# Kernel optimization log

Hardware: AMD Instinct MI355X
Metric: run time of the kernel (lower is better)

The kernel has to match this reference:

```python
import jax, jax.numpy as jnp
import numpy as np

D = 64        # in_out_dim
M = 512       # hidden_dim
N = 4096      # batch
R = 10        # rank of quadratic term A (min(10, d+1))
ALPHA0 = 1.0  # alpha[0]
H = 1.0       # ResNet step h = 1/(nTh-1), nTh=2


def antideriv_tanh(x):
    # log(2*cosh(x)), numerically stable antiderivative of tanh
    ax = jnp.abs(x)
    return ax + jnp.log1p(jnp.exp(-2.0 * ax))


def setup_inputs() -> dict:
    key = jax.random.key(0)
    ks = jax.random.split(key, 10)
    f32 = jnp.float32
    return {
        "x":   jax.random.normal(ks[0], (N, D), f32),
        "t":   jax.random.uniform(ks[1], (), f32),
        "K0":  jax.random.normal(ks[2], (M, D + 1), f32) * (1.0 / np.sqrt(D + 1)),
        "b0":  jax.random.normal(ks[3], (M,), f32) * 0.1,
        "K1":  jax.random.normal(ks[4], (M, M), f32) * (1.0 / np.sqrt(M)),
        "b1":  jax.random.normal(ks[5], (M,), f32) * 0.1,
        "w":   jax.random.normal(ks[6], (M,), f32) * (1.0 / np.sqrt(M)),
        "A":   jax.random.normal(ks[7], (R, D + 1), f32) * (1.0 / np.sqrt(D + 1)),
        "c_w": jax.random.normal(ks[8], (D + 1,), f32) * 0.1,
        "c_b": jax.random.normal(ks[9], (), f32) * 0.1,
    }


def _tr_hess(s, K0, b0, K1, b1, w, A, c_w):
    # s: [N, d+1]; analytic gradient + Hessian trace of the OT-Flow potential.
    d = s.shape[1] - 1
    symA = A.T @ A                                   # [d+1, d+1]

    # forward through ResNet (nTh=2 -> one residual layer)
    opening = s @ K0.T + b0                          # [N, m]
    u0 = antideriv_tanh(opening)                     # [N, m]
    lin1 = u0 @ K1.T + b1                            # [N, m]

    tanh_open = jnp.tanh(opening)
    tanh_lin1 = jnp.tanh(lin1)

    # backward z-chain for the gradient
    z1 = w + H * (tanh_lin1 * w) @ K1                # [N, m]
    z0 = (tanh_open * z1) @ K0                       # [N, d+1]
    grad = z0 + s @ symA + c_w                       # [N, d+1]

    # trace of Hessian w.r.t. the first d coordinates
    Kopen = K0[:, :d]                                # [m, d]
    dt_open = 1.0 - tanh_open ** 2
    trH = (dt_open * z1) @ jnp.sum(Kopen ** 2, axis=1)          # [N]
    Jac = tanh_open[:, :, None] * Kopen[None]                    # [N, m, d]
    KJ = jnp.einsum('ij,njk->nik', K1, Jac)                      # [N, m, d]
    dt_lin1 = 1.0 - tanh_lin1 ** 2
    t1 = jnp.einsum('nj,njk->n', dt_lin1 * w, KJ ** 2)           # [N]
    trH = trH + H * t1 + jnp.trace(symA[:d, :d])
    return grad, trH


def reference(x, t, K0, b0, K1, b1, w, A, c_w, c_b):
    n = x.shape[0]
    s = jnp.concatenate([x, jnp.ones((n, 1), x.dtype) * t], axis=1)  # pad time
    gradPhi, trH = _tr_hess(s, K0, b0, K1, b1, w, A, c_w)
    dPhi_dx = gradPhi[:, :D]                         # [N, d]
    dPhi_dt = gradPhi[:, D:D + 1]                    # [N, 1]
    dz_dt = -(1.0 / ALPHA0) * dPhi_dx
    dlogp_dt = -(1.0 / ALPHA0) * trH[:, None]
    cost_L_dt = 0.5 * jnp.sum(dz_dt ** 2, axis=1, keepdims=True)
    cost_HJB_dt = jnp.abs(-dPhi_dt + ALPHA0 * cost_L_dt)
    return (dz_dt, dlogp_dt, cost_L_dt, cost_HJB_dt)
```

## Files before the change

### kernel.cpp

```cpp
#include <hip/hip_runtime.h>
#include <stdint.h>

#define D_  64
#define DP1 65
#define M_  512
#define N_  4096

typedef float f32x4 __attribute__((ext_vector_type(4)));
typedef _Float16 h8 __attribute__((ext_vector_type(8)));

__global__ void prepk(const float* __restrict__ A, const float* __restrict__ K0,
                      const float* __restrict__ K1, const float* __restrict__ x,
                      const float* __restrict__ tptr, const float* __restrict__ b0,
                      float* symA, float* sumK2,
                      _Float16* K1h, _Float16* K1Th, _Float16* K0Th,
                      _Float16* u0h, _Float16* ah, float* trH0){
  __shared__ float shm[2*64*66];
  int b = blockIdx.x;
  int t = threadIdx.x;
  if (b == 0){
    for (int idx = t; idx < DP1*DP1; idx += 256){
      int e = idx / DP1, d = idx % DP1;
      float s = 0.f;
      for (int r = 0; r < 10; ++r) s += A[r*DP1+e]*A[r*DP1+d];
      symA[idx] = s;
    }
    for (int m = t; m < M_; m += 256){
      float s = 0.f;
      for (int k = 0; k < D_; ++k){ float v = K0[m*DP1+k]; s += v*v; }
      sumK2[m] = s;
    }
  } else if (b < 65){
    int bb = b - 1;
    int r0 = (bb>>3)*64, c0 = (bb&7)*64;
    float* tile = shm;
    for (int it = 0; it < 16; ++it){
      int lin = it*256 + t;
      int r = lin >> 6, c = lin & 63;
      float v = K1[(r0+r)*M_ + c0+c];
      tile[r*65+c] = v;
      K1h[(r0+r)*M_ + c0+c] = (_Float16)v;
    }
    __syncthreads();
    for (int it = 0; it < 16; ++it){
      int lin = it*256 + t;
      int r = lin >> 6, c = lin & 63;
      K1Th[(c0+r)*M_ + (r0+c)] = (_Float16)tile[c*65+r];
    }
  } else if (b < 225){
    int idx = (b-65)*256 + t;
    if (idx < 80*M_){
      int d = idx / M_, i = idx % M_;
      float v = (d < DP1) ? K0[i*DP1 + d] : 0.f;
      K0Th[idx] = (_Float16)v;
    }
  } else {
    int bb = b - 225;
    int n0 = (bb & 63)*64, m0 = (bb >> 6)*64;
    float* sS = shm;
    float* sK = shm + 64*66;
    float tval = tptr[0];
    for (int it = 0; it < 17; ++it){
      int lin = it*256 + t;
      if (lin < 64*65){
        int r = lin/65, c = lin%65;
        sS[r*66+c] = (c < 64) ? x[(n0+r)*64 + c] : tval;
        sK[r*66+c] = K0[(m0+r)*DP1 + c];
      }
    }
    __syncthreads();
    int tn = (t>>4)*4, tm = (t&15)*4;
    float acc[4][4] = {};
    for (int e = 0; e < DP1; ++e){
      float sv[4], kv[4];
      for (int i=0;i<4;++i){ sv[i]=sS[(tn+i)*66+e]; kv[i]=sK[(tm+i)*66+e]; }
      for (int i=0;i<4;++i) for(int j=0;j<4;++j) acc[i][j] += sv[i]*kv[j];
    }
    for (int i=0;i<4;++i) for(int j=0;j<4;++j){
      int n = n0+tn+i, m = m0+tm+j;
      float o = acc[i][j] + b0[m];
      float a = tanhf(o);
      float ax = fabsf(o);
      float u0 = ax + log1pf(expf(-2.f*ax));
      u0h[n*M_+m] = (_Float16)u0;
      ah[n*M_+m]  = (_Float16)a;
    }
    if (m0 == 0 && t < 64) trH0[n0+t] = 0.f;
  }
}

template<int MODE>
__launch_bounds__(256, 2)
__global__ void gemm512(const _Float16* __restrict__ Ah, const _Float16* __restrict__ Wh,
                        const float* __restrict__ bias, const float* __restrict__ w,
                        const _Float16* __restrict__ ah, const float* __restrict__ sumK2,
                        _Float16* out0, _Float16* out1, float* trH0){
  __shared__ _Float16 sW[64*512];
  int n0 = blockIdx.x*64, i0 = blockIdx.y*64;
  int t = threadIdx.x;
  int wv = t>>6, l = t&63;
  int c15 = l & 15, g = l>>4;
  h8 af[16];
  {
    const _Float16* ap = Ah + (size_t)(n0 + wv*16 + c15)*M_ + g*8;
    #pragma unroll
    for (int tt = 0; tt < 16; ++tt) af[tt] = *(const h8*)(ap + tt*32);
  }
  #pragma unroll
  for (int it = 0; it < 16; ++it){
    int r = it*4 + wv;
    const _Float16* src = Wh + (size_t)(i0 + r)*M_ + ((l ^ (r & 7))*8);
    __builtin_amdgcn_global_load_lds(
        (const __attribute__((address_space(1))) void*)src,
        (__attribute__((address_space(3))) void*)(&sW[r*512]), 16, 0, 0);
  }
  __syncthreads();
  f32x4 zero = {0.f,0.f,0.f,0.f};
  f32x4 acc[4]; for (int k=0;k<4;++k) acc[k]=zero;
  #pragma unroll
  for (int step = 0; step < 16; ++step){
    int p0 = (((step*4 + g) ^ (c15 & 7))*8);
    h8 bf0 = *(const h8*)(&sW[(     c15)*512 + p0]);
    h8 bf1 = *(const h8*)(&sW[(16 + c15)*512 + p0]);
    h8 bf2 = *(const h8*)(&sW[(32 + c15)*512 + p0]);
    h8 bf3 = *(const h8*)(&sW[(48 + c15)*512 + p0]);
    h8 a = af[step];
    acc[0] = __builtin_amdgcn_mfma_f32_16x16x32_f16(a, bf0, acc[0], 0, 0, 0);
    acc[1] = __builtin_amdgcn_mfma_f32_16x16x32_f16(a, bf1, acc[1], 0, 0, 0);
    acc[2] = __builtin_amdgcn_mfma_f32_16x16x32_f16(a, bf2, acc[2], 0, 0, 0);
    acc[3] = __builtin_amdgcn_mfma_f32_16x16x32_f16(a, bf3, acc[3], 0, 0, 0);
  }
  if (MODE == 0){
    for (int kt=0;kt<4;++kt) for (int r=0;r<4;++r){
      int n = n0+wv*16+(l>>4)*4+r;
      int i = i0+kt*16+c15;
      float v = acc[kt][r] + bias[i];
      float tl = tanhf(v);
      out0[n*M_+i] = (_Float16)(tl*w[i]);
      out1[n*M_+i] = (_Float16)((1.f-tl*tl)*w[i]);
    }
  } else {
    for (int r=0;r<4;++r){
      int n = n0+wv*16+(l>>4)*4+r;
      float rowpart = 0.f;
      for (int kt=0;kt<4;++kt){
        int i = i0+kt*16+c15;
        float z1 = acc[kt][r] + w[i];
        float a = (float)ah[n*M_+i];
        out0[n*M_+i] = (_Float16)(a*z1);
        rowpart += (1.f-a*a)*z1*sumK2[i];
      }
      for (int m=1;m<16;m<<=1) rowpart += __shfl_xor(rowpart, m);
      if (c15==0) atomicAdd(&trH0[n], rowpart);
    }
  }
}

__launch_bounds__(256, 4)
__global__ void gemmz0(const _Float16* __restrict__ az1h, const _Float16* __restrict__ K0Th,
                       float* z0p){
  int n0 = blockIdx.x*64;
  int q  = blockIdx.y;
  int t = threadIdx.x, wv = t>>6, l = t&63;
  int r15 = l & 15;
  int krow = q*128 + (l>>4)*8;
  const _Float16* abase = az1h + (size_t)(n0 + wv*16 + r15)*M_ + krow;
  const _Float16* kb0 = K0Th + (size_t)( 0 + r15)*M_ + krow;
  const _Float16* kb1 = K0Th + (size_t)(16 + r15)*M_ + krow;
  const _Float16* kb2 = K0Th + (size_t)(32 + r15)*M_ + krow;
  const _Float16* kb3 = K0Th + (size_t)(48 + r15)*M_ + krow;
  const _Float16* kb4 = K0Th + (size_t)(64 + r15)*M_ + krow;
  f32x4 zero = {0.f,0.f,0.f,0.f};
  f32x4 acc[5]; for (int k=0;k<5;++k) acc[k]=zero;
  #pragma unroll
  for (int ii = 0; ii < 4; ++ii){
    const int j0 = ii*32;
    h8 af = *(const h8*)(abase + j0);
    h8 b0c = *(const h8*)(kb0 + j0);
    h8 b1c = *(const h8*)(kb1 + j0);
    h8 b2c = *(const h8*)(kb2 + j0);
    h8 b3c = *(const h8*)(kb3 + j0);
    h8 b4c = *(const h8*)(kb4 + j0);
    acc[0] = __builtin_amdgcn_mfma_f32_16x16x32_f16(af, b0c, acc[0], 0, 0, 0);
    acc[1] = __builtin_amdgcn_mfma_f32_16x16x32_f16(af, b1c, acc[1], 0, 0, 0);
    acc[2] = __builtin_amdgcn_mfma_f32_16x16x32_f16(af, b2c, acc[2], 0, 0, 0);
    acc[3] = __builtin_amdgcn_mfma_f32_16x16x32_f16(af, b3c, acc[3], 0, 0, 0);
    acc[4] = __builtin_amdgcn_mfma_f32_16x16x32_f16(af, b4c, acc[4], 0, 0, 0);
  }
  float* zp = z0p + (size_t)q*N_*80;
  for (int dt=0; dt<5; ++dt) for (int r=0;r<4;++r){
    int n = n0+wv*16+(l>>4)*4+r;
    int d = dt*16+r15;
    zp[n*80+d] = acc[dt][r];
  }
}

__launch_bounds__(256, 2)
__global__ void kjk13(const _Float16* __restrict__ K1h, const _Float16* __restrict__ K0Th,
                      const _Float16* __restrict__ ah, const _Float16* __restrict__ ch,
                      float* trH0){
  __shared__ _Float16 sK1[64*512];
  __shared__ _Float16 sAv[8*512];
  int t = threadIdx.x;
  int n0 = blockIdx.x*8;
  int i0 = blockIdx.y*64;
  int wv = t>>6, l = t&63;
  int c15 = l & 15, g = l>>4;
  h8 kf[16];
  {
    const _Float16* kfp = K0Th + (size_t)(wv*16 + c15)*M_ + g*8;
    #pragma unroll
    for (int tt = 0; tt < 16; ++tt) kf[tt] = *(const h8*)(kfp + tt*32);
  }
  #pragma unroll
  for (int it = 0; it < 16; ++it){
    int r = it*4 + wv;
    const _Float16* src = K1h + (size_t)(i0 + r)*M_ + ((l ^ (r & 7))*8);
    __builtin_amdgcn_global_load_lds(
        (const __attribute__((address_space(1))) void*)src,
        (__attribute__((address_space(3))) void*)(&sK1[r*512]), 16, 0, 0);
  }
  #pragma unroll
  for (int it = 0; it < 2; ++it){
    int cc = it*256 + t;
    int s = cc >> 6, c = cc & 63;
    *(h8*)(&sAv[s*512 + c*8]) = *(const h8*)(ah + (size_t)(n0+s)*M_ + c*8);
  }
  __syncthreads();
  f32x4 zero = {0.f,0.f,0.f,0.f};
  f32x4 acc[4][8];
  #pragma unroll
  for (int tt=0;tt<4;++tt)
    #pragma unroll
    for (int s=0;s<8;++s) acc[tt][s]=zero;
  #pragma unroll
  for (int step = 0; step < 16; ++step){
    int p0 = (((step*4 + g) ^ (c15 & 7))*8);
    h8 bf0 = *(const h8*)(&sK1[(     c15)*512 + p0]);
    h8 bf1 = *(const h8*)(&sK1[(16 + c15)*512 + p0]);
    h8 bf2 = *(const h8*)(&sK1[(32 + c15)*512 + p0]);
    h8 bf3 = *(const h8*)(&sK1[(48 + c15)*512 + p0]);
    int aoff = step*32 + g*8;
    h8 k = kf[step];
    #pragma unroll
    for (int s = 0; s < 8; ++s){
      h8 av = *(const h8*)(&sAv[s*512 + aoff]);
      h8 ap = k*av;
      acc[0][s] = __builtin_amdgcn_mfma_f32_16x16x32_f16(ap, bf0, acc[0][s], 0, 0, 0);
      acc[1][s] = __builtin_amdgcn_mfma_f32_16x16x32_f16(ap, bf1, acc[1][s], 0, 0, 0);
      acc[2][s] = __builtin_amdgcn_mfma_f32_16x16x32_f16(ap, bf2, acc[2][s], 0, 0, 0);
      acc[3][s] = __builtin_amdgcn_mfma_f32_16x16x32_f16(ap, bf3, acc[3][s], 0, 0, 0);
    }
  }
  #pragma unroll
  for (int s = 0; s < 8; ++s){
    float part = 0.f;
    #pragma unroll
    for (int tt = 0; tt < 4; ++tt){
      float ci = (float)ch[(size_t)(n0+s)*M_ + i0 + tt*16 + c15];
      f32x4 a = acc[tt][s];
      part += ci*(a[0]*a[0] + a[1]*a[1] + a[2]*a[2] + a[3]*a[3]);
    }
    for (int m=32;m>=1;m>>=1) part += __shfl_xor(part, m);
    if (l == 0) atomicAdd(&trH0[n0+s], part);
  }
}

__global__ void finalk(const float* __restrict__ x, const float* __restrict__ tptr,
                       const float* __restrict__ symA, const float* __restrict__ c_w,
                       const float* __restrict__ z0p, const float* __restrict__ trH0,
                       float* out){
  __shared__ float sA[DP1*DP1];
  int t = threadIdx.x;
  for (int i = t; i < DP1*DP1; i += 256) sA[i] = symA[i];
  __syncthreads();
  int wv = t>>6, l = t&63;
  int n = blockIdx.x*4 + wv;
  float tval = tptr[0];
  float sv = x[n*64 + l];
  float z0l = z0p[(size_t)0*N_*80 + n*80 + l] + z0p[(size_t)1*N_*80 + n*80 + l]
            + z0p[(size_t)2*N_*80 + n*80 + l] + z0p[(size_t)3*N_*80 + n*80 + l];
  float z0t = z0p[(size_t)0*N_*80 + n*80 + 64] + z0p[(size_t)1*N_*80 + n*80 + 64]
            + z0p[(size_t)2*N_*80 + n*80 + 64] + z0p[(size_t)3*N_*80 + n*80 + 64];
  float acc = z0l + c_w[l];
  for (int e = 0; e < 64; ++e){
    float se = __shfl(sv, e);
    acc += se * sA[l*DP1 + e];
  }
  acc += tval * sA[l*DP1 + 64];
  float trd = sA[l*66];
  for (int m=32;m>=1;m>>=1) trd += __shfl_xor(trd, m);
  float g64 = sv * sA[64*DP1 + l];
  for (int m=32;m>=1;m>>=1) g64 += __shfl_xor(g64, m);
  g64 += tval*sA[64*DP1+64] + z0t + c_w[64];
  float dz = -acc;
  out[n*64 + l] = dz;
  float q = dz*dz;
  for (int m=32;m>=1;m>>=1) q += __shfl_xor(q, m);
  float costL = 0.5f*q;
  if (l == 0){
    out[N_*64 + n]        = -(trH0[n] + trd);
    out[N_*64 + N_ + n]   = costL;
    out[N_*64 + 2*N_ + n] = fabsf(-g64 + costL);
  }
}

extern "C" void kernel_launch(void* const* d_in, const int* in_sizes, int n_in,
                              void* d_out, int out_size, void* d_ws, size_t ws_size,
                              hipStream_t stream){
  const float* x   = (const float*)d_in[0];
  const float* tp  = (const float*)d_in[1];
  const float* K0  = (const float*)d_in[2];
  const float* b0  = (const float*)d_in[3];
  const float* K1  = (const float*)d_in[4];
  const float* b1  = (const float*)d_in[5];
  const float* w   = (const float*)d_in[6];
  const float* A   = (const float*)d_in[7];
  const float* c_w = (const float*)d_in[8];
  float* out = (float*)d_out;

  char* ws = (char*)d_ws;
  size_t off = 0;
  auto alloc = [&](size_t bytes)->void*{
    void* p = ws + off; off += bytes; off = (off + 255) & ~(size_t)255; return p;
  };
  _Float16* K1h   = (_Float16*)alloc(512*512*2);
  _Float16* K1Th  = (_Float16*)alloc(512*512*2);
  _Float16* K0Th  = (_Float16*)alloc(80*512*2);
  float* symA     = (float*)alloc(DP1*DP1*4);
  float* sumK2    = (float*)alloc(512*4);
  _Float16* u0h   = (_Float16*)alloc((size_t)N_*M_*2);
  _Float16* ah    = (_Float16*)alloc((size_t)N_*M_*2);
  _Float16* tl1wh = (_Float16*)alloc((size_t)N_*M_*2);
  _Float16* ch    = (_Float16*)alloc((size_t)N_*M_*2);
  _Float16* az1h  = (_Float16*)alloc((size_t)N_*M_*2);
  float* z0p      = (float*)alloc((size_t)4*N_*80*4);
  float* trH0     = (float*)alloc(N_*4);

  prepk<<<737, 256, 0, stream>>>(A, K0, K1, x, tp, b0, symA, sumK2,
                                 K1h, K1Th, K0Th, u0h, ah, trH0);
  gemm512<0><<<dim3(N_/64, M_/64), 256, 0, stream>>>(u0h, K1h, b1, w, nullptr, nullptr,
                                                     tl1wh, ch, nullptr);
  gemm512<1><<<dim3(N_/64, M_/64), 256, 0, stream>>>(tl1wh, K1Th, nullptr, w, ah, sumK2,
                                                     az1h, nullptr, trH0);
  gemmz0<<<dim3(N_/64, 4), 256, 0, stream>>>(az1h, K0Th, z0p);
  kjk13<<<dim3(N_/8, 8), 256, 0, stream>>>(K1h, K0Th, ah, ch, trH0);
  finalk<<<N_/4, 256, 0, stream>>>(x, tp, symA, c_w, z0p, trH0, out);
}
```

Baseline: 193.0 us.

## Merge second GEMM with KJ trace kernel and fold z0 GEMM into final kernel

The independent gemm512<1> and kjk13 launches become one combined grid, with block index choosing the role, so their work can overlap on the GPU. The separate gemmz0 MFMA kernel and its partial-sum buffer are removed. finalk now computes z0 itself as scalar fp16 dot products over the 512-wide hidden dimension. This removes two launches and the z0p round trip, but moves a 4096x512x65 product from MFMA onto per-lane scalar loops that read K0Th rows with a poor access pattern.

```diff
diff --git a/kernel.cpp b/kernel.cpp
--- a/kernel.cpp
+++ b/kernel.cpp
@@ -89,12 +89,10 @@
   }
 }
 
-template<int MODE>
 __launch_bounds__(256, 2)
-__global__ void gemm512(const _Float16* __restrict__ Ah, const _Float16* __restrict__ Wh,
-                        const float* __restrict__ bias, const float* __restrict__ w,
-                        const _Float16* __restrict__ ah, const float* __restrict__ sumK2,
-                        _Float16* out0, _Float16* out1, float* trH0){
+__global__ void gemm0(const _Float16* __restrict__ Ah, const _Float16* __restrict__ Wh,
+                      const float* __restrict__ bias, const float* __restrict__ w,
+                      _Float16* out0, _Float16* out1){
   __shared__ _Float16 sW[64*512];
   int n0 = blockIdx.x*64, i0 = blockIdx.y*64;
   int t = threadIdx.x;
@@ -130,16 +128,124 @@
     acc[2] = __builtin_amdgcn_mfma_f32_16x16x32_f16(a, bf2, acc[2], 0, 0, 0);
     acc[3] = __builtin_amdgcn_mfma_f32_16x16x32_f16(a, bf3, acc[3], 0, 0, 0);
   }
-  if (MODE == 0){
-    for (int kt=0;kt<4;++kt) for (int r=0;r<4;++r){
-      int n = n0+wv*16+(l>>4)*4+r;
-      int i = i0+kt*16+c15;
-      float v = acc[kt][r] + bias[i];
-      float tl = tanhf(v);
-      out0[n*M_+i] = (_Float16)(tl*w[i]);
-      out1[n*M_+i] = (_Float16)((1.f-tl*tl)*w[i]);
+  for (int kt=0;kt<4;++kt) for (int r=0;r<4;++r){
+    int n = n0+wv*16+(l>>4)*4+r;
+    int i = i0+kt*16+c15;
+    float v = acc[kt][r] + bias[i];
+    float tl = tanhf(v);
+    out0[n*M_+i] = (_Float16)(tl*w[i]);
+    out1[n*M_+i] = (_Float16)((1.f-tl*tl)*w[i]);
+  }
+}
+
+__launch_bounds__(256, 2)
+__global__ void g1kjk(const _Float16* __restrict__ tl1wh, const _Float16* __restrict__ K1Th,
+                      const _Float16* __restrict__ K1h, const _Float16* __restrict__ K0Th,
+                      const _Float16* __restrict__ ah, const _Float16* __restrict__ ch,
+                      const float* __restrict__ w, const float* __restrict__ sumK2,
+                      _Float16* az1h, float* trH0){
+  __shared__ _Float16 shm[64*512 + 8*512];
+  int b = blockIdx.x;
+  int t = threadIdx.x;
+  int wv = t>>6, l = t&63;
+  int c15 = l & 15, g = l>>4;
+  if (b < 4096){
+    _Float16* sK1 = shm;
+    _Float16* sAv = shm + 64*512;
+    int n0 = (b>>3)*8;
+    int i0 = (b&7)*64;
+    h8 kf[16];
+    {
+      const _Float16* kfp = K0Th + (size_t)(wv*16 + c15)*M_ + g*8;
+      #pragma unroll
+      for (int tt = 0; tt < 16; ++tt) kf[tt] = *(const h8*)(kfp + tt*32);
+    }
+    #pragma unroll
+    for (int it = 0; it < 16; ++it){
+      int r = it*4 + wv;
+      const _Float16* src = K1h + (size_t)(i0 + r)*M_ + ((l ^ (r & 7))*8);
+      __builtin_amdgcn_global_load_lds(
+          (const __attribute__((address_space(1))) void*)src,
+          (__attribute__((address_space(3))) void*)(&sK1[r*512]), 16, 0, 0);
+    }
+    #pragma unroll
+    for (int it = 0; it < 2; ++it){
+      int cc = it*256 + t;
+      int s = cc >> 6, c = cc & 63;
+      *(h8*)(&sAv[s*512 + c*8]) = *(const h8*)(ah + (size_t)(n0+s)*M_ + c*8);
+    }
+    __syncthreads();
+    f32x4 zero = {0.f,0.f,0.f,0.f};
+    f32x4 acc[4][8];
+    #pragma unroll
+    for (int tt=0;tt<4;++tt)
+      #pragma unroll
+      for (int s=0;s<8;++s) acc[tt][s]=zero;
+    #pragma unroll
+    for (int step = 0; step < 16; ++step){
+      int p0 = (((step*4 + g) ^ (c15 & 7))*8);
+      h8 bf0 = *(const h8*)(&sK1[(     c15)*512 + p0]);
+      h8 bf1 = *(const h8*)(&sK1[(16 + c15)*512 + p0]);
+      h8 bf2 = *(const h8*)(&sK1[(32 + c15)*512 + p0]);
+      h8 bf3 = *(const h8*)(&sK1[(48 + c15)*512 + p0]);
+      int aoff = step*32 + g*8;
+      h8 k = kf[step];
+      #pragma unroll
+      for (int s = 0; s < 8; ++s){
+        h8 av = *(const h8*)(&sAv[s*512 + aoff]);
+        h8 ap = k*av;
+        acc[0][s] = __builtin_amdgcn_mfma_f32_16x16x32_f16(ap, bf0, acc[0][s], 0, 0, 0);
+        acc[1][s] = __builtin_amdgcn_mfma_f32_16x16x32_f16(ap, bf1, acc[1][s], 0, 0, 0);
+        acc[2][s] = __builtin_amdgcn_mfma_f32_16x16x32_f16(ap, bf2, acc[2][s], 0, 0, 0);
+        acc[3][s] = __builtin_amdgcn_mfma_f32_16x16x32_f16(ap, bf3, acc[3][s], 0, 0, 0);
+      }
+    }
+    #pragma unroll
+    for (int s = 0; s < 8; ++s){
+      float part = 0.f;
+      #pragma unroll
+      for (int tt = 0; tt < 4; ++tt){
+        float ci = (float)ch[(size_t)(n0+s)*M_ + i0 + tt*16 + c15];
+        f32x4 a = acc[tt][s];
+        part += ci*(a[0]*a[0] + a[1]*a[1] + a[2]*a[2] + a[3]*a[3]);
+      }
+      for (int m=32;m>=1;m>>=1) part += __shfl_xor(part, m);
+      if (l == 0) atomicAdd(&trH0[n0+s], part);
     }
   } else {
+    _Float16* sW = shm;
+    int bb = b - 4096;
+    int n0 = (bb>>3)*64, i0 = (bb&7)*64;
+    h8 af[16];
+    {
+      const _Float16* ap = tl1wh + (size_t)(n0 + wv*16 + c15)*M_ + g*8;
+      #pragma unroll
+      for (int tt = 0; tt < 16; ++tt) af[tt] = *(const h8*)(ap + tt*32);
+    }
+    #pragma unroll
+    for (int it = 0; it < 16; ++it){
+      int r = it*4 + wv;
+      const _Float16* src = K1Th + (size_t)(i0 + r)*M_ + ((l ^ (r & 7))*8);
+      __builtin_amdgcn_global_load_lds(
+          (const __attribute__((address_space(1))) void*)src,
+          (__attribute__((address_space(3))) void*)(&sW[r*512]), 16, 0, 0);
+    }
+    __syncthreads();
+    f32x4 zero = {0.f,0.f,0.f,0.f};
+    f32x4 acc[4]; for (int k=0;k<4;++k) acc[k]=zero;
+    #pragma unroll
+    for (int step = 0; step < 16; ++step){
+      int p0 = (((step*4 + g) ^ (c15 & 7))*8);
+      h8 bf0 = *(const h8*)(&sW[(     c15)*512 + p0]);
+      h8 bf1 = *(const h8*)(&sW[(16 + c15)*512 + p0]);
+      h8 bf2 = *(const h8*)(&sW[(32 + c15)*512 + p0]);
+      h8 bf3 = *(const h8*)(&sW[(48 + c15)*512 + p0]);
+      h8 a = af[step];
+      acc[0] = __builtin_amdgcn_mfma_f32_16x16x32_f16(a, bf0, acc[0], 0, 0, 0);
+      acc[1] = __builtin_amdgcn_mfma_f32_16x16x32_f16(a, bf1, acc[1], 0, 0, 0);
+      acc[2] = __builtin_amdgcn_mfma_f32_16x16x32_f16(a, bf2, acc[2], 0, 0, 0);
+      acc[3] = __builtin_amdgcn_mfma_f32_16x16x32_f16(a, bf3, acc[3], 0, 0, 0);
+    }
     for (int r=0;r<4;++r){
       int n = n0+wv*16+(l>>4)*4+r;
       float rowpart = 0.f;
@@ -147,7 +253,7 @@
         int i = i0+kt*16+c15;
         float z1 = acc[kt][r] + w[i];
         float a = (float)ah[n*M_+i];
-        out0[n*M_+i] = (_Float16)(a*z1);
+        az1h[n*M_+i] = (_Float16)(a*z1);
         rowpart += (1.f-a*a)*z1*sumK2[i];
       }
       for (int m=1;m<16;m<<=1) rowpart += __shfl_xor(rowpart, m);
@@ -156,120 +262,10 @@
   }
 }
 
-__launch_bounds__(256, 4)
-__global__ void gemmz0(const _Float16* __restrict__ az1h, const _Float16* __restrict__ K0Th,
-                       float* z0p){
-  int n0 = blockIdx.x*64;
-  int q  = blockIdx.y;
-  int t = threadIdx.x, wv = t>>6, l = t&63;
-  int r15 = l & 15;
-  int krow = q*128 + (l>>4)*8;
-  const _Float16* abase = az1h + (size_t)(n0 + wv*16 + r15)*M_ + krow;
-  const _Float16* kb0 = K0Th + (size_t)( 0 + r15)*M_ + krow;
-  const _Float16* kb1 = K0Th + (size_t)(16 + r15)*M_ + krow;
-  const _Float16* kb2 = K0Th + (size_t)(32 + r15)*M_ + krow;
-  const _Float16* kb3 = K0Th + (size_t)(48 + r15)*M_ + krow;
-  const _Float16* kb4 = K0Th + (size_t)(64 + r15)*M_ + krow;
-  f32x4 zero = {0.f,0.f,0.f,0.f};
-  f32x4 acc[5]; for (int k=0;k<5;++k) acc[k]=zero;
-  #pragma unroll
-  for (int ii = 0; ii < 4; ++ii){
-    const int j0 = ii*32;
-    h8 af = *(const h8*)(abase + j0);
-    h8 b0c = *(const h8*)(kb0 + j0);
-    h8 b1c = *(const h8*)(kb1 + j0);
-    h8 b2c = *(const h8*)(kb2 + j0);
-    h8 b3c = *(const h8*)(kb3 + j0);
-    h8 b4c = *(const h8*)(kb4 + j0);
-    acc[0] = __builtin_amdgcn_mfma_f32_16x16x32_f16(af, b0c, acc[0], 0, 0, 0);
-    acc[1] = __builtin_amdgcn_mfma_f32_16x16x32_f16(af, b1c, acc[1], 0, 0, 0);
-    acc[2] = __builtin_amdgcn_mfma_f32_16x16x32_f16(af, b2c, acc[2], 0, 0, 0);
-    acc[3] = __builtin_amdgcn_mfma_f32_16x16x32_f16(af, b3c, acc[3], 0, 0, 0);
-    acc[4] = __builtin_amdgcn_mfma_f32_16x16x32_f16(af, b4c, acc[4], 0, 0, 0);
-  }
-  float* zp = z0p + (size_t)q*N_*80;
-  for (int dt=0; dt<5; ++dt) for (int r=0;r<4;++r){
-    int n = n0+wv*16+(l>>4)*4+r;
-    int d = dt*16+r15;
-    zp[n*80+d] = acc[dt][r];
-  }
-}
-
-__launch_bounds__(256, 2)
-__global__ void kjk13(const _Float16* __restrict__ K1h, const _Float16* __restrict__ K0Th,
-                      const _Float16* __restrict__ ah, const _Float16* __restrict__ ch,
-                      float* trH0){
-  __shared__ _Float16 sK1[64*512];
-  __shared__ _Float16 sAv[8*512];
-  int t = threadIdx.x;
-  int n0 = blockIdx.x*8;
-  int i0 = blockIdx.y*64;
-  int wv = t>>6, l = t&63;
-  int c15 = l & 15, g = l>>4;
-  h8 kf[16];
-  {
-    const _Float16* kfp = K0Th + (size_t)(wv*16 + c15)*M_ + g*8;
-    #pragma unroll
-    for (int tt = 0; tt < 16; ++tt) kf[tt] = *(const h8*)(kfp + tt*32);
-  }
-  #pragma unroll
-  for (int it = 0; it < 16; ++it){
-    int r = it*4 + wv;
-    const _Float16* src = K1h + (size_t)(i0 + r)*M_ + ((l ^ (r & 7))*8);
-    __builtin_amdgcn_global_load_lds(
-        (const __attribute__((address_space(1))) void*)src,
-        (__attribute__((address_space(3))) void*)(&sK1[r*512]), 16, 0, 0);
-  }
-  #pragma unroll
-  for (int it = 0; it < 2; ++it){
-    int cc = it*256 + t;
-    int s = cc >> 6, c = cc & 63;
-    *(h8*)(&sAv[s*512 + c*8]) = *(const h8*)(ah + (size_t)(n0+s)*M_ + c*8);
-  }
-  __syncthreads();
-  f32x4 zero = {0.f,0.f,0.f,0.f};
-  f32x4 acc[4][8];
-  #pragma unroll
-  for (int tt=0;tt<4;++tt)
-    #pragma unroll
-    for (int s=0;s<8;++s) acc[tt][s]=zero;
-  #pragma unroll
-  for (int step = 0; step < 16; ++step){
-    int p0 = (((step*4 + g) ^ (c15 & 7))*8);
-    h8 bf0 = *(const h8*)(&sK1[(     c15)*512 + p0]);
-    h8 bf1 = *(const h8*)(&sK1[(16 + c15)*512 + p0]);
-    h8 bf2 = *(const h8*)(&sK1[(32 + c15)*512 + p0]);
-    h8 bf3 = *(const h8*)(&sK1[(48 + c15)*512 + p0]);
-    int aoff = step*32 + g*8;
-    h8 k = kf[step];
-    #pragma unroll
-    for (int s = 0; s < 8; ++s){
-      h8 av = *(const h8*)(&sAv[s*512 + aoff]);
-      h8 ap = k*av;
-      acc[0][s] = __builtin_amdgcn_mfma_f32_16x16x32_f16(ap, bf0, acc[0][s], 0, 0, 0);
-      acc[1][s] = __builtin_amdgcn_mfma_f32_16x16x32_f16(ap, bf1, acc[1][s], 0, 0, 0);
-      acc[2][s] = __builtin_amdgcn_mfma_f32_16x16x32_f16(ap, bf2, acc[2][s], 0, 0, 0);
-      acc[3][s] = __builtin_amdgcn_mfma_f32_16x16x32_f16(ap, bf3, acc[3][s], 0, 0, 0);
-    }
-  }
-  #pragma unroll
-  for (int s = 0; s < 8; ++s){
-    float part = 0.f;
-    #pragma unroll
-    for (int tt = 0; tt < 4; ++tt){
-      float ci = (float)ch[(size_t)(n0+s)*M_ + i0 + tt*16 + c15];
-      f32x4 a = acc[tt][s];
-      part += ci*(a[0]*a[0] + a[1]*a[1] + a[2]*a[2] + a[3]*a[3]);
-    }
-    for (int m=32;m>=1;m>>=1) part += __shfl_xor(part, m);
-    if (l == 0) atomicAdd(&trH0[n0+s], part);
-  }
-}
-
 __global__ void finalk(const float* __restrict__ x, const float* __restrict__ tptr,
                        const float* __restrict__ symA, const float* __restrict__ c_w,
-                       const float* __restrict__ z0p, const float* __restrict__ trH0,
-                       float* out){
+                       const _Float16* __restrict__ az1h, const _Float16* __restrict__ K0Th,
+                       const float* __restrict__ trH0, float* out){
   __shared__ float sA[DP1*DP1];
   int t = threadIdx.x;
   for (int i = t; i < DP1*DP1; i += 256) sA[i] = symA[i];
@@ -278,10 +274,24 @@
   int n = blockIdx.x*4 + wv;
   float tval = tptr[0];
   float sv = x[n*64 + l];
-  float z0l = z0p[(size_t)0*N_*80 + n*80 + l] + z0p[(size_t)1*N_*80 + n*80 + l]
-            + z0p[(size_t)2*N_*80 + n*80 + l] + z0p[(size_t)3*N_*80 + n*80 + l];
-  float z0t = z0p[(size_t)0*N_*80 + n*80 + 64] + z0p[(size_t)1*N_*80 + n*80 + 64]
-            + z0p[(size_t)2*N_*80 + n*80 + 64] + z0p[(size_t)3*N_*80 + n*80 + 64];
+  const _Float16* az = az1h + (size_t)n*M_;
+  const _Float16* kr = K0Th + (size_t)l*M_;
+  float z0l = 0.f;
+  for (int c = 0; c < 64; ++c){
+    h8 a = *(const h8*)(az + c*8);
+    h8 k = *(const h8*)(kr + c*8);
+    #pragma unroll
+    for (int e = 0; e < 8; ++e) z0l += (float)a[e]*(float)k[e];
+  }
+  float z0t = 0.f;
+  {
+    const _Float16* k64 = K0Th + (size_t)64*M_;
+    h8 a = *(const h8*)(az + l*8);
+    h8 k = *(const h8*)(k64 + l*8);
+    #pragma unroll
+    for (int e = 0; e < 8; ++e) z0t += (float)a[e]*(float)k[e];
+    for (int m=32;m>=1;m>>=1) z0t += __shfl_xor(z0t, m);
+  }
   float acc = z0l + c_w[l];
   for (int e = 0; e < 64; ++e){
     float se = __shfl(sv, e);
@@ -334,16 +344,12 @@
   _Float16* tl1wh = (_Float16*)alloc((size_t)N_*M_*2);
   _Float16* ch    = (_Float16*)alloc((size_t)N_*M_*2);
   _Float16* az1h  = (_Float16*)alloc((size_t)N_*M_*2);
-  float* z0p      = (float*)alloc((size_t)4*N_*80*4);
   float* trH0     = (float*)alloc(N_*4);
 
   prepk<<<737, 256, 0, stream>>>(A, K0, K1, x, tp, b0, symA, sumK2,
                                  K1h, K1Th, K0Th, u0h, ah, trH0);
-  gemm512<0><<<dim3(N_/64, M_/64), 256, 0, stream>>>(u0h, K1h, b1, w, nullptr, nullptr,
-                                                     tl1wh, ch, nullptr);
-  gemm512<1><<<dim3(N_/64, M_/64), 256, 0, stream>>>(tl1wh, K1Th, nullptr, w, ah, sumK2,
-                                                     az1h, nullptr, trH0);
-  gemmz0<<<dim3(N_/64, 4), 256, 0, stream>>>(az1h, K0Th, z0p);
-  kjk13<<<dim3(N_/8, 8), 256, 0, stream>>>(K1h, K0Th, ah, ch, trH0);
-  finalk<<<N_/4, 256, 0, stream>>>(x, tp, symA, c_w, z0p, trH0, out);
-}
+  gemm0<<<dim3(N_/64, M_/64), 256, 0, stream>>>(u0h, K1h, b1, w, tl1wh, ch);
+  g1kjk<<<4608, 256, 0, stream>>>(tl1wh, K1Th, K1h, K0Th, ah, ch, w, sumK2,
+                                  az1h, trH0);
+  finalk<<<N_/4, 256, 0, stream>>>(x, tp, symA, c_w, az1h, K0Th, trH0, out);
+}
```

Result: slower. 258.3 us (+33.8%).

## Split Hessian-trace kernel across 8 waves with fewer samples per block

Applied to the files above, without the earlier changes.

The KJ² trace kernel now launches 512-thread blocks that each handle 4 samples instead of 8. The 64-row K1 tile is split into two 32-row halves across wave pairs, and the K0 fragments are loaded in two halves. This cuts per-thread accumulator and fragment registers to raise occupancy and hide MFMA and LDS latency. In exchange, each K1 tile staged into LDS is reused across half as many samples, which doubles global/L2 traffic for K1.

```diff
diff --git a/kernel.cpp b/kernel.cpp
--- a/kernel.cpp
+++ b/kernel.cpp
@@ -195,69 +195,80 @@
   }
 }
 
-__launch_bounds__(256, 2)
-__global__ void kjk13(const _Float16* __restrict__ K1h, const _Float16* __restrict__ K0Th,
+__launch_bounds__(512, 4)
+__global__ void kjk14(const _Float16* __restrict__ K1h, const _Float16* __restrict__ K0Th,
                       const _Float16* __restrict__ ah, const _Float16* __restrict__ ch,
                       float* trH0){
   __shared__ _Float16 sK1[64*512];
-  __shared__ _Float16 sAv[8*512];
+  __shared__ _Float16 sAv[4*512];
   int t = threadIdx.x;
-  int n0 = blockIdx.x*8;
+  int n0 = blockIdx.x*4;
   int i0 = blockIdx.y*64;
   int wv = t>>6, l = t&63;
   int c15 = l & 15, g = l>>4;
-  h8 kf[16];
-  {
-    const _Float16* kfp = K0Th + (size_t)(wv*16 + c15)*M_ + g*8;
-    #pragma unroll
-    for (int tt = 0; tt < 16; ++tt) kf[tt] = *(const h8*)(kfp + tt*32);
-  }
-  #pragma unroll
-  for (int it = 0; it < 16; ++it){
-    int r = it*4 + wv;
+  int ih = (wv&1)*32;
+  int ks = wv>>1;
+  const _Float16* kfp = K0Th + (size_t)(ks*16 + c15)*M_ + g*8;
+  h8 kf[8];
+  #pragma unroll
+  for (int st = 0; st < 8; ++st) kf[st] = *(const h8*)(kfp + st*32);
+  #pragma unroll
+  for (int it = 0; it < 8; ++it){
+    int r = it*8 + wv;
     const _Float16* src = K1h + (size_t)(i0 + r)*M_ + ((l ^ (r & 7))*8);
     __builtin_amdgcn_global_load_lds(
         (const __attribute__((address_space(1))) void*)src,
         (__attribute__((address_space(3))) void*)(&sK1[r*512]), 16, 0, 0);
   }
-  #pragma unroll
-  for (int it = 0; it < 2; ++it){
-    int cc = it*256 + t;
-    int s = cc >> 6, c = cc & 63;
+  if (t < 256){
+    int s = t>>6, c = t&63;
     *(h8*)(&sAv[s*512 + c*8]) = *(const h8*)(ah + (size_t)(n0+s)*M_ + c*8);
   }
   __syncthreads();
   f32x4 zero = {0.f,0.f,0.f,0.f};
-  f32x4 acc[4][8];
-  #pragma unroll
-  for (int tt=0;tt<4;++tt)
-    #pragma unroll
-    for (int s=0;s<8;++s) acc[tt][s]=zero;
-  #pragma unroll
-  for (int step = 0; step < 16; ++step){
+  f32x4 acc[2][4];
+  #pragma unroll
+  for (int tt=0;tt<2;++tt)
+    #pragma unroll
+    for (int s=0;s<4;++s) acc[tt][s]=zero;
+  #pragma unroll
+  for (int step = 0; step < 8; ++step){
     int p0 = (((step*4 + g) ^ (c15 & 7))*8);
-    h8 bf0 = *(const h8*)(&sK1[(     c15)*512 + p0]);
-    h8 bf1 = *(const h8*)(&sK1[(16 + c15)*512 + p0]);
-    h8 bf2 = *(const h8*)(&sK1[(32 + c15)*512 + p0]);
-    h8 bf3 = *(const h8*)(&sK1[(48 + c15)*512 + p0]);
+    h8 bf0 = *(const h8*)(&sK1[(ih +      c15)*512 + p0]);
+    h8 bf1 = *(const h8*)(&sK1[(ih + 16 + c15)*512 + p0]);
     int aoff = step*32 + g*8;
     h8 k = kf[step];
     #pragma unroll
-    for (int s = 0; s < 8; ++s){
+    for (int s = 0; s < 4; ++s){
       h8 av = *(const h8*)(&sAv[s*512 + aoff]);
       h8 ap = k*av;
       acc[0][s] = __builtin_amdgcn_mfma_f32_16x16x32_f16(ap, bf0, acc[0][s], 0, 0, 0);
       acc[1][s] = __builtin_amdgcn_mfma_f32_16x16x32_f16(ap, bf1, acc[1][s], 0, 0, 0);
-      acc[2][s] = __builtin_amdgcn_mfma_f32_16x16x32_f16(ap, bf2, acc[2][s], 0, 0, 0);
-      acc[3][s] = __builtin_amdgcn_mfma_f32_16x16x32_f16(ap, bf3, acc[3][s], 0, 0, 0);
-    }
-  }
-  #pragma unroll
-  for (int s = 0; s < 8; ++s){
+    }
+  }
+  #pragma unroll
+  for (int st = 0; st < 8; ++st) kf[st] = *(const h8*)(kfp + (st+8)*32);
+  #pragma unroll
+  for (int step = 8; step < 16; ++step){
+    int p0 = (((step*4 + g) ^ (c15 & 7))*8);
+    h8 bf0 = *(const h8*)(&sK1[(ih +      c15)*512 + p0]);
+    h8 bf1 = *(const h8*)(&sK1[(ih + 16 + c15)*512 + p0]);
+    int aoff = step*32 + g*8;
+    h8 k = kf[step-8];
+    #pragma unroll
+    for (int s = 0; s < 4; ++s){
+      h8 av = *(const h8*)(&sAv[s*512 + aoff]);
+      h8 ap = k*av;
+      acc[0][s] = __builtin_amdgcn_mfma_f32_16x16x32_f16(ap, bf0, acc[0][s], 0, 0, 0);
+      acc[1][s] = __builtin_amdgcn_mfma_f32_16x16x32_f16(ap, bf1, acc[1][s], 0, 0, 0);
+    }
+  }
+  #pragma unroll
+  for (int s = 0; s < 4; ++s){
     float part = 0.f;
     #pragma unroll
-    for (int tt = 0; tt < 4; ++tt){
-      float ci = (float)ch[(size_t)(n0+s)*M_ + i0 + tt*16 + c15];
+    for (int tt = 0; tt < 2; ++tt){
+      float ci = (float)ch[(size_t)(n0+s)*M_ + i0 + ih + tt*16 + c15];
       f32x4 a = acc[tt][s];
       part += ci*(a[0]*a[0] + a[1]*a[1] + a[2]*a[2] + a[3]*a[3]);
     }
@@ -344,6 +355,6 @@
   gemm512<1><<<dim3(N_/64, M_/64), 256, 0, stream>>>(tl1wh, K1Th, nullptr, w, ah, sumK2,
                                                      az1h, nullptr, trH0);
   gemmz0<<<dim3(N_/64, 4), 256, 0, stream>>>(az1h, K0Th, z0p);
-  kjk13<<<dim3(N_/8, 8), 256, 0, stream>>>(K1h, K0Th, ah, ch, trH0);
+  kjk14<<<dim3(N_/4, 8), 512, 0, stream>>>(K1h, K0Th, ah, ch, trH0);
   finalk<<<N_/4, 256, 0, stream>>>(x, tp, symA, c_w, z0p, trH0, out);
 }
```

Result: slower. 263.4 us (+36.4%).
